# Performance work log

Hardware: AMD Instinct MI355X
Metric: run time of the kernel (lower is better)

The kernel has to match this reference:

```python
import jax, jax.numpy as jnp
import numpy as np

N, D = 8192, 128
WEIGHT = 0.01


def _neg_flat_indices(n):
    # Replicates: mask = ones(n,n); fill_diagonal_(0); mask[i,i+1]=0; mask[i+1,i]=0
    # i.e. keep (i,j) with j != i, j != i+1, j != i-1. Row-major flatnonzero
    # reproduces torch's sim[mask] flattening order exactly.
    i = np.arange(n)[:, None]
    j = np.arange(n)[None, :]
    mask = (j != i) & (j != i + 1) & (j != i - 1)
    idx = np.flatnonzero(mask)
    assert idx.size == (n - 1) * (n - 2)
    return idx


NEG_IDX = jnp.asarray(_neg_flat_indices(N))  # [(N-1)*(N-2)] int32/int64 constant


def setup_inputs() -> dict:
    key = jax.random.key(0)
    factor = jax.random.normal(key, (N, D), dtype=jnp.float32)
    return {"factor": factor}


def reference(factor):
    n = factor.shape[0]
    # F.normalize(factor): L2-normalize rows with eps=1e-12
    norms = jnp.linalg.norm(factor, axis=1, keepdims=True)
    f = factor / jnp.maximum(norms, 1e-12)
    sim = f @ f.T                                   # [N, N] gram matrix
    pos = jnp.diagonal(sim, offset=1).reshape(n - 1, 1)      # [N-1, 1]
    neg = sim.reshape(-1)[NEG_IDX].reshape(n - 1, n - 2)     # [N-1, N-2]
    logits = jnp.concatenate([pos, neg], axis=1)             # [N-1, N-1]
    # CrossEntropyLoss(reduction='sum') with all-zero labels:
    # sum_i (logsumexp(logits_i) - logits_i[0])
    loss = jnp.sum(jax.nn.logsumexp(logits, axis=1) - logits[:, 0])
    loss = loss / n
    return -WEIGHT * loss
```

## Files before the change

### kernel.cpp

```cpp
#include <hip/hip_runtime.h>
#include <hip/hip_bf16.h>

#define N 8192
#define D 128
#define WEIGHT 0.01f
#define NTILES 64
#define NBLK 2080

typedef __bf16 bf16x8 __attribute__((ext_vector_type(8)));
typedef float floatx4 __attribute__((ext_vector_type(4)));

__global__ __launch_bounds__(256) void k_norm(const float* __restrict__ x,
                                              __hip_bfloat16* __restrict__ fb,
                                              float* __restrict__ out) {
    int gid = blockIdx.x * 256 + threadIdx.x;
    if (gid == 0) out[0] = 0.0f;
    int row = gid >> 4;
    int c   = gid & 15;
    const float4* xr = (const float4*)(x + (size_t)row * D + c * 8);
    float4 f0 = xr[0], f1 = xr[1];
    float s = f0.x * f0.x + f0.y * f0.y + f0.z * f0.z + f0.w * f0.w
            + f1.x * f1.x + f1.y * f1.y + f1.z * f1.z + f1.w * f1.w;
    s += __shfl_xor(s, 1, 64);
    s += __shfl_xor(s, 2, 64);
    s += __shfl_xor(s, 4, 64);
    s += __shfl_xor(s, 8, 64);
    float inv = 1.0f / fmaxf(sqrtf(s), 1e-12f);
    union { __hip_bfloat16 h[8]; uint4 u; } pk;
    pk.h[0] = __float2bfloat16(f0.x * inv);
    pk.h[1] = __float2bfloat16(f0.y * inv);
    pk.h[2] = __float2bfloat16(f0.z * inv);
    pk.h[3] = __float2bfloat16(f0.w * inv);
    pk.h[4] = __float2bfloat16(f1.x * inv);
    pk.h[5] = __float2bfloat16(f1.y * inv);
    pk.h[6] = __float2bfloat16(f1.z * inv);
    pk.h[7] = __float2bfloat16(f1.w * inv);
    ((uint4*)fb)[(size_t)row * 16 + (c ^ (row & 15))] = pk.u;
}

__global__ __launch_bounds__(256, 2) void k_gram(const __hip_bfloat16* __restrict__ fb,
                                                 float* __restrict__ Prow,
                                                 float* __restrict__ Pcol,
                                                 float* __restrict__ p,
                                                 float* __restrict__ ep) {
    int b = blockIdx.x;
    int bi = (int)((2.0 * NTILES + 1.0 - sqrt((2.0 * NTILES + 1.0) * (2.0 * NTILES + 1.0) - 8.0 * (double)b)) * 0.5);
    while (bi * NTILES - bi * (bi - 1) / 2 > b) --bi;
    while ((bi + 1) * NTILES - (bi + 1) * bi / 2 <= b) ++bi;
    int bj = bi + (b - (bi * NTILES - bi * (bi - 1) / 2));

    __shared__ uint4 Ab[2048];
    __shared__ uint4 Bb[2048];
    __shared__ float PR[2][128];
    __shared__ float PC[2][128];

    const int t = threadIdx.x;
    const int lane = t & 63;
    const int wid  = t >> 6;
    const int wrow = wid >> 1, wcol = wid & 1;
    const int col0 = lane & 15;
    const int quad = lane >> 4;
    const int rbase = bi * 128, cbase = bj * 128;

    const uint4* gA = (const uint4*)fb + (size_t)rbase * 16;
    const uint4* gB = (const uint4*)fb + (size_t)cbase * 16;
    #pragma unroll
    for (int i = 0; i < 8; ++i) {
        int ca = wid * 512 + i * 64;
        __builtin_amdgcn_global_load_lds(
            (const __attribute__((address_space(1))) void*)(gA + ca + lane),
            (__attribute__((address_space(3))) void*)&Ab[ca], 16, 0, 0);
        __builtin_amdgcn_global_load_lds(
            (const __attribute__((address_space(1))) void*)(gB + ca + lane),
            (__attribute__((address_space(3))) void*)&Bb[ca], 16, 0, 0);
    }
    __syncthreads();

    floatx4 acc[4][4];
    #pragma unroll
    for (int a = 0; a < 4; ++a)
        #pragma unroll
        for (int c = 0; c < 4; ++c)
            acc[a][c] = (floatx4){0.0f, 0.0f, 0.0f, 0.0f};

    #pragma unroll
    for (int ks = 0; ks < 4; ++ks) {
        bf16x8 af[4], bfr[4];
        int j = ks * 4 + quad;
        int jsw = j ^ col0;
        #pragma unroll
        for (int mt = 0; mt < 4; ++mt) {
            int rl = wrow * 64 + mt * 16 + col0;
            af[mt] = *(const bf16x8*)&Ab[rl * 16 + jsw];
        }
        #pragma unroll
        for (int nt = 0; nt < 4; ++nt) {
            int cl = wcol * 64 + nt * 16 + col0;
            bfr[nt] = *(const bf16x8*)&Bb[cl * 16 + jsw];
        }
        #pragma unroll
        for (int mt = 0; mt < 4; ++mt)
            #pragma unroll
            for (int nt = 0; nt < 4; ++nt)
                acc[mt][nt] = __builtin_amdgcn_mfma_f32_16x16x32_bf16(af[mt], bfr[nt], acc[mt][nt], 0, 0, 0);
    }

    float v[16];
    float colpart[4];
    #pragma unroll
    for (int m = 0; m < 16; ++m) v[m] = 0.0f;
    #pragma unroll
    for (int m = 0; m < 4; ++m) colpart[m] = 0.0f;

    if (bj > bi + 1) {
        #pragma unroll
        for (int mt = 0; mt < 4; ++mt)
            #pragma unroll
            for (int nt = 0; nt < 4; ++nt)
                #pragma unroll
                for (int reg = 0; reg < 4; ++reg) {
                    float e = __expf(acc[mt][nt][reg]);
                    v[mt * 4 + reg] += e;
                    colpart[nt] += e;
                }
    } else {
        #pragma unroll
        for (int mt = 0; mt < 4; ++mt)
            #pragma unroll
            for (int nt = 0; nt < 4; ++nt)
                #pragma unroll
                for (int reg = 0; reg < 4; ++reg) {
                    int r = rbase + wrow * 64 + mt * 16 + quad * 4 + reg;
                    int c = cbase + wcol * 64 + nt * 16 + col0;
                    float s0 = acc[mt][nt][reg];
                    float e = __expf(s0);
                    if (c == r + 1) { p[r] = s0; ep[r] = e; }
                    e = (c > r) ? e : 0.0f;
                    v[mt * 4 + reg] += e;
                    colpart[nt] += e;
                }
    }

    float v8[8];
    #pragma unroll
    for (int k = 0; k < 8; ++k) {
        float a = v[2 * k], bb = v[2 * k + 1];
        float give = (lane & 1) ? a : bb;
        float keep = (lane & 1) ? bb : a;
        v8[k] = keep + __shfl_xor(give, 1, 64);
    }
    float v4[4];
    #pragma unroll
    for (int k = 0; k < 4; ++k) {
        float a = v8[2 * k], bb = v8[2 * k + 1];
        float give = (lane & 2) ? a : bb;
        float keep = (lane & 2) ? bb : a;
        v4[k] = keep + __shfl_xor(give, 2, 64);
    }
    float v2[2];
    #pragma unroll
    for (int k = 0; k < 2; ++k) {
        float a = v4[2 * k], bb = v4[2 * k + 1];
        float give = (lane & 4) ? a : bb;
        float keep = (lane & 4) ? bb : a;
        v2[k] = keep + __shfl_xor(give, 4, 64);
    }
    {
        float a = v2[0], bb = v2[1];
        float give = (lane & 8) ? a : bb;
        float keep = (lane & 8) ? bb : a;
        float v1 = keep + __shfl_xor(give, 8, 64);
        int rowl = wrow * 64 + (col0 >> 2) * 16 + quad * 4 + (col0 & 3);
        PR[wcol][rowl] = v1;
    }
    {
        float c2[2];
        #pragma unroll
        for (int k = 0; k < 2; ++k) {
            float a = colpart[2 * k];
            float bb = colpart[2 * k + 1];
            float give = (lane & 16) ? a : bb;
            float keep = (lane & 16) ? bb : a;
            c2[k] = keep + __shfl_xor(give, 16, 64);
        }
        float a = c2[0], bb = c2[1];
        float give = (lane & 32) ? a : bb;
        float keep = (lane & 32) ? bb : a;
        float cv = keep + __shfl_xor(give, 32, 64);
        PC[wrow][wcol * 64 + lane] = cv;
    }
    __syncthreads();

    if (t < 128) {
        Prow[(size_t)b * 128 + t] = PR[0][t] + PR[1][t];
    } else {
        int c = t - 128;
        Pcol[(size_t)b * 128 + c] = PC[0][c] + PC[1][c];
    }
}

__global__ __launch_bounds__(256) void k_tail(const float* __restrict__ Prow,
                                              const float* __restrict__ Pcol,
                                              const float* __restrict__ p,
                                              const float* __restrict__ ep,
                                              float* __restrict__ out) {
    __shared__ float Ush[128];
    __shared__ float Lsh[128];
    __shared__ float sw[4];
    int band = blockIdx.x;
    int t = threadIdx.x;
    if (t < 128) {
        int baseU = band * NTILES - band * (band - 1) / 2;
        float s = 0.0f;
        for (int bj = band; bj < NTILES; ++bj)
            s += Prow[(size_t)(baseU + bj - band) * 128 + t];
        Ush[t] = s;
    } else {
        int c = band * 128 + (t - 128) + 1;
        float s = 0.0f;
        if (c < N) {
            int bc = c >> 7;
            for (int bi = 0; bi <= bc; ++bi)
                s += Pcol[(size_t)(bi * NTILES - bi * (bi - 1) / 2 + (bc - bi)) * 128 + (c & 127)];
        }
        Lsh[t - 128] = s;
    }
    __syncthreads();
    float term = 0.0f;
    if (t < 128) {
        int r = band * 128 + t;
        if (r < N - 1)
            term = __logf(Ush[t] + Lsh[t] - ep[r]) - p[r];
    }
    #pragma unroll
    for (int m = 1; m < 64; m <<= 1) term += __shfl_xor(term, m, 64);
    int lane = t & 63, wd = t >> 6;
    if (lane == 0) sw[wd] = term;
    __syncthreads();
    if (t == 0) {
        float part = sw[0] + sw[1] + sw[2] + sw[3];
        atomicAdd(out, -WEIGHT * part / (float)N);
    }
}

extern "C" void kernel_launch(void* const* d_in, const int* in_sizes, int n_in,
                              void* d_out, int out_size, void* d_ws, size_t ws_size,
                              hipStream_t stream) {
    const float* x = (const float*)d_in[0];
    float* out = (float*)d_out;
    char* ws = (char*)d_ws;
    __hip_bfloat16* fb = (__hip_bfloat16*)ws;
    float* p    = (float*)(ws + (size_t)N * D * 2);
    float* ep   = p + N;
    float* Prow = ep + N;
    float* Pcol = Prow + (size_t)NBLK * 128;

    hipLaunchKernelGGL(k_norm, dim3(512),  dim3(256), 0, stream, x, fb, out);
    hipLaunchKernelGGL(k_gram, dim3(NBLK), dim3(256), 0, stream, fb, Prow, Pcol, p, ep);
    hipLaunchKernelGGL(k_tail, dim3(64),   dim3(256), 0, stream, Prow, Pcol, p, ep, out);
}
```

Before: 95.33 us.

## Fuse tail reduction into gram kernel via atomic ticket and spin barrier

Drops the separate k_tail launch. Each gram block takes an atomic ticket after writing its partials. The last 64 ticket holders wait on a flag set by the final block, then each does one band's reduction and adds to the output. This removes a kernel launch and its gap, at the cost of an atomic per block and spin-waiting blocks, which could delay the final block's scheduling.

```diff
diff --git a/kernel.cpp b/kernel.cpp
--- a/kernel.cpp
+++ b/kernel.cpp
@@ -6,15 +6,17 @@
 #define WEIGHT 0.01f
 #define NTILES 64
 #define NBLK 2080
+#define NTAIL 64
 
 typedef __bf16 bf16x8 __attribute__((ext_vector_type(8)));
 typedef float floatx4 __attribute__((ext_vector_type(4)));
 
 __global__ __launch_bounds__(256) void k_norm(const float* __restrict__ x,
                                               __hip_bfloat16* __restrict__ fb,
-                                              float* __restrict__ out) {
+                                              float* __restrict__ out,
+                                              unsigned* __restrict__ sync) {
     int gid = blockIdx.x * 256 + threadIdx.x;
-    if (gid == 0) out[0] = 0.0f;
+    if (gid == 0) { out[0] = 0.0f; sync[0] = 0u; sync[32] = 0u; }
     int row = gid >> 4;
     int c   = gid & 15;
     const float4* xr = (const float4*)(x + (size_t)row * D + c * 8);
@@ -42,7 +44,9 @@
                                                  float* __restrict__ Prow,
                                                  float* __restrict__ Pcol,
                                                  float* __restrict__ p,
-                                                 float* __restrict__ ep) {
+                                                 float* __restrict__ ep,
+                                                 unsigned* __restrict__ sync,
+                                                 float* __restrict__ out) {
     int b = blockIdx.x;
     int bi = (int)((2.0 * NTILES + 1.0 - sqrt((2.0 * NTILES + 1.0) * (2.0 * NTILES + 1.0) - 8.0 * (double)b)) * 0.5);
     while (bi * NTILES - bi * (bi - 1) / 2 > b) --bi;
@@ -53,6 +57,7 @@
     __shared__ uint4 Bb[2048];
     __shared__ float PR[2][128];
     __shared__ float PC[2][128];
+    __shared__ unsigned ticket_sh;
 
     const int t = threadIdx.x;
     const int lane = t & 63;
@@ -197,49 +202,58 @@
         int c = t - 128;
         Pcol[(size_t)b * 128 + c] = PC[0][c] + PC[1][c];
     }
-}
-
-__global__ __launch_bounds__(256) void k_tail(const float* __restrict__ Prow,
-                                              const float* __restrict__ Pcol,
-                                              const float* __restrict__ p,
-                                              const float* __restrict__ ep,
-                                              float* __restrict__ out) {
-    __shared__ float Ush[128];
-    __shared__ float Lsh[128];
-    __shared__ float sw[4];
-    int band = blockIdx.x;
-    int t = threadIdx.x;
-    if (t < 128) {
-        int baseU = band * NTILES - band * (band - 1) / 2;
-        float s = 0.0f;
-        for (int bj = band; bj < NTILES; ++bj)
-            s += Prow[(size_t)(baseU + bj - band) * 128 + t];
-        Ush[t] = s;
+
+    __threadfence();
+    __syncthreads();
+    if (t == 0)
+        ticket_sh = __hip_atomic_fetch_add(&sync[0], 1u, __ATOMIC_ACQ_REL, __HIP_MEMORY_SCOPE_AGENT);
+    __syncthreads();
+    unsigned ticket = ticket_sh;
+    if (ticket < NBLK - NTAIL) return;
+
+    if (ticket == NBLK - 1) {
+        if (t == 0)
+            __hip_atomic_store(&sync[32], 1u, __ATOMIC_RELEASE, __HIP_MEMORY_SCOPE_AGENT);
     } else {
-        int c = band * 128 + (t - 128) + 1;
-        float s = 0.0f;
-        if (c < N) {
-            int bc = c >> 7;
-            for (int bi = 0; bi <= bc; ++bi)
-                s += Pcol[(size_t)(bi * NTILES - bi * (bi - 1) / 2 + (bc - bi)) * 128 + (c & 127)];
-        }
-        Lsh[t - 128] = s;
-    }
-    __syncthreads();
-    float term = 0.0f;
-    if (t < 128) {
-        int r = band * 128 + t;
-        if (r < N - 1)
-            term = __logf(Ush[t] + Lsh[t] - ep[r]) - p[r];
-    }
-    #pragma unroll
-    for (int m = 1; m < 64; m <<= 1) term += __shfl_xor(term, m, 64);
-    int lane = t & 63, wd = t >> 6;
-    if (lane == 0) sw[wd] = term;
-    __syncthreads();
-    if (t == 0) {
-        float part = sw[0] + sw[1] + sw[2] + sw[3];
-        atomicAdd(out, -WEIGHT * part / (float)N);
+        if (t == 0)
+            while (__hip_atomic_load(&sync[32], __ATOMIC_ACQUIRE, __HIP_MEMORY_SCOPE_AGENT) == 0u)
+                __builtin_amdgcn_s_sleep(4);
+        __syncthreads();
+    }
+
+    {
+        int band = (int)ticket - (NBLK - NTAIL);
+        if (t < 128) {
+            int baseU = band * NTILES - band * (band - 1) / 2;
+            float s = 0.0f;
+            for (int bjj = band; bjj < NTILES; ++bjj)
+                s += Prow[(size_t)(baseU + bjj - band) * 128 + t];
+            PR[0][t] = s;
+        } else {
+            int c = band * 128 + (t - 128) + 1;
+            float s = 0.0f;
+            if (c < N) {
+                int bc = c >> 7;
+                for (int bii = 0; bii <= bc; ++bii)
+                    s += Pcol[(size_t)(bii * NTILES - bii * (bii - 1) / 2 + (bc - bii)) * 128 + (c & 127)];
+            }
+            PR[1][t - 128] = s;
+        }
+        __syncthreads();
+        float term = 0.0f;
+        if (t < 128) {
+            int r = band * 128 + t;
+            if (r < N - 1)
+                term = __logf(PR[0][t] + PR[1][t] - ep[r]) - p[r];
+        }
+        #pragma unroll
+        for (int m = 1; m < 64; m <<= 1) term += __shfl_xor(term, m, 64);
+        if (lane == 0) PC[0][wid] = term;
+        __syncthreads();
+        if (t == 0) {
+            float part = PC[0][0] + PC[0][1] + PC[0][2] + PC[0][3];
+            atomicAdd(out, -WEIGHT * part / (float)N);
+        }
     }
 }
 
@@ -252,10 +266,10 @@
     __hip_bfloat16* fb = (__hip_bfloat16*)ws;
     float* p    = (float*)(ws + (size_t)N * D * 2);
     float* ep   = p + N;
-    float* Prow = ep + N;
+    unsigned* sync = (unsigned*)(ep + N);
+    float* Prow = (float*)(sync + 64);
     float* Pcol = Prow + (size_t)NBLK * 128;
 
-    hipLaunchKernelGGL(k_norm, dim3(512),  dim3(256), 0, stream, x, fb, out);
-    hipLaunchKernelGGL(k_gram, dim3(NBLK), dim3(256), 0, stream, fb, Prow, Pcol, p, ep);
-    hipLaunchKernelGGL(k_tail, dim3(64),   dim3(256), 0, stream, Prow, Pcol, p, ep, out);
+    hipLaunchKernelGGL(k_norm, dim3(512),  dim3(256), 0, stream, x, fb, out, sync);
+    hipLaunchKernelGGL(k_gram, dim3(NBLK), dim3(256), 0, stream, fb, Prow, Pcol, p, ep, sync, out);
 }
```

Result: slower. 271.2 us (+184.5%).

## Switch normalized features and gram MFMA from bf16 to fp8 e4m3

Applied to the files above, without the earlier changes.

Normalized rows are now quantized to fp8 e4m3 instead of bf16, which halves the staged operand bytes and LDS tile size. The gram kernel uses the fp8 16x16x32 MFMA with a new 8-byte swizzle layout, and occupancy is raised to 4 blocks per CU. The aim is to cut MFMA time and memory traffic in the gram stage, at the cost of much lower precision in the similarities that feed exp/logsumexp, which risks failing the accuracy tolerance.

```diff
diff --git a/kernel.cpp b/kernel.cpp
--- a/kernel.cpp
+++ b/kernel.cpp
@@ -1,5 +1,6 @@
 #include <hip/hip_runtime.h>
 #include <hip/hip_bf16.h>
+#include <hip/hip_fp8.h>
 
 #define N 8192
 #define D 128
@@ -7,11 +8,10 @@
 #define NTILES 64
 #define NBLK 2080
 
-typedef __bf16 bf16x8 __attribute__((ext_vector_type(8)));
 typedef float floatx4 __attribute__((ext_vector_type(4)));
 
 __global__ __launch_bounds__(256) void k_norm(const float* __restrict__ x,
-                                              __hip_bfloat16* __restrict__ fb,
+                                              unsigned char* __restrict__ fb8,
                                               float* __restrict__ out) {
     int gid = blockIdx.x * 256 + threadIdx.x;
     if (gid == 0) out[0] = 0.0f;
@@ -26,19 +26,20 @@
     s += __shfl_xor(s, 4, 64);
     s += __shfl_xor(s, 8, 64);
     float inv = 1.0f / fmaxf(sqrtf(s), 1e-12f);
-    union { __hip_bfloat16 h[8]; uint4 u; } pk;
-    pk.h[0] = __float2bfloat16(f0.x * inv);
-    pk.h[1] = __float2bfloat16(f0.y * inv);
-    pk.h[2] = __float2bfloat16(f0.z * inv);
-    pk.h[3] = __float2bfloat16(f0.w * inv);
-    pk.h[4] = __float2bfloat16(f1.x * inv);
-    pk.h[5] = __float2bfloat16(f1.y * inv);
-    pk.h[6] = __float2bfloat16(f1.z * inv);
-    pk.h[7] = __float2bfloat16(f1.w * inv);
-    ((uint4*)fb)[(size_t)row * 16 + (c ^ (row & 15))] = pk.u;
-}
-
-__global__ __launch_bounds__(256, 2) void k_gram(const __hip_bfloat16* __restrict__ fb,
+    union { unsigned char b[8]; uint2 u; } pk;
+    pk.b[0] = __hip_fp8_e4m3(f0.x * inv).__x;
+    pk.b[1] = __hip_fp8_e4m3(f0.y * inv).__x;
+    pk.b[2] = __hip_fp8_e4m3(f0.z * inv).__x;
+    pk.b[3] = __hip_fp8_e4m3(f0.w * inv).__x;
+    pk.b[4] = __hip_fp8_e4m3(f1.x * inv).__x;
+    pk.b[5] = __hip_fp8_e4m3(f1.y * inv).__x;
+    pk.b[6] = __hip_fp8_e4m3(f1.z * inv).__x;
+    pk.b[7] = __hip_fp8_e4m3(f1.w * inv).__x;
+    int cc = c >> 1, h = c & 1;
+    ((uint2*)fb8)[(size_t)row * 16 + (((cc ^ (row & 7)) << 1) | h)] = pk.u;
+}
+
+__global__ __launch_bounds__(256, 4) void k_gram(const unsigned char* __restrict__ fb8,
                                                  float* __restrict__ Prow,
                                                  float* __restrict__ Pcol,
                                                  float* __restrict__ p,
@@ -49,8 +50,8 @@
     while ((bi + 1) * NTILES - (bi + 1) * bi / 2 <= b) ++bi;
     int bj = bi + (b - (bi * NTILES - bi * (bi - 1) / 2));
 
-    __shared__ uint4 Ab[2048];
-    __shared__ uint4 Bb[2048];
+    __shared__ uint4 Ab[1024];
+    __shared__ uint4 Bb[1024];
     __shared__ float PR[2][128];
     __shared__ float PC[2][128];
 
@@ -62,11 +63,11 @@
     const int quad = lane >> 4;
     const int rbase = bi * 128, cbase = bj * 128;
 
-    const uint4* gA = (const uint4*)fb + (size_t)rbase * 16;
-    const uint4* gB = (const uint4*)fb + (size_t)cbase * 16;
-    #pragma unroll
-    for (int i = 0; i < 8; ++i) {
-        int ca = wid * 512 + i * 64;
+    const uint4* gA = (const uint4*)fb8 + (size_t)rbase * 8;
+    const uint4* gB = (const uint4*)fb8 + (size_t)cbase * 8;
+    #pragma unroll
+    for (int i = 0; i < 4; ++i) {
+        int ca = wid * 256 + i * 64;
         __builtin_amdgcn_global_load_lds(
             (const __attribute__((address_space(1))) void*)(gA + ca + lane),
             (__attribute__((address_space(3))) void*)&Ab[ca], 16, 0, 0);
@@ -83,26 +84,30 @@
         for (int c = 0; c < 4; ++c)
             acc[a][c] = (floatx4){0.0f, 0.0f, 0.0f, 0.0f};
 
+    const long* A8 = (const long*)Ab;
+    const long* B8 = (const long*)Bb;
+    const int swz = (col0 & 7);
     #pragma unroll
     for (int ks = 0; ks < 4; ++ks) {
-        bf16x8 af[4], bfr[4];
-        int j = ks * 4 + quad;
-        int jsw = j ^ col0;
+        long af[4], bfr[4];
+        int cc = ks * 2 + (quad >> 1);
+        int off = quad & 1;
+        int base8 = ((cc ^ swz) << 1) | off;
         #pragma unroll
         for (int mt = 0; mt < 4; ++mt) {
             int rl = wrow * 64 + mt * 16 + col0;
-            af[mt] = *(const bf16x8*)&Ab[rl * 16 + jsw];
+            af[mt] = A8[rl * 16 + base8];
         }
         #pragma unroll
         for (int nt = 0; nt < 4; ++nt) {
             int cl = wcol * 64 + nt * 16 + col0;
-            bfr[nt] = *(const bf16x8*)&Bb[cl * 16 + jsw];
+            bfr[nt] = B8[cl * 16 + base8];
         }
         #pragma unroll
         for (int mt = 0; mt < 4; ++mt)
             #pragma unroll
             for (int nt = 0; nt < 4; ++nt)
-                acc[mt][nt] = __builtin_amdgcn_mfma_f32_16x16x32_bf16(af[mt], bfr[nt], acc[mt][nt], 0, 0, 0);
+                acc[mt][nt] = __builtin_amdgcn_mfma_f32_16x16x32_fp8_fp8(af[mt], bfr[nt], acc[mt][nt], 0, 0, 0);
     }
 
     float v[16];
@@ -249,13 +254,13 @@
     const float* x = (const float*)d_in[0];
     float* out = (float*)d_out;
     char* ws = (char*)d_ws;
-    __hip_bfloat16* fb = (__hip_bfloat16*)ws;
-    float* p    = (float*)(ws + (size_t)N * D * 2);
+    unsigned char* fb8 = (unsigned char*)ws;
+    float* p    = (float*)(ws + (size_t)N * D);
     float* ep   = p + N;
     float* Prow = ep + N;
     float* Pcol = Prow + (size_t)NBLK * 128;
 
-    hipLaunchKernelGGL(k_norm, dim3(512),  dim3(256), 0, stream, x, fb, out);
-    hipLaunchKernelGGL(k_gram, dim3(NBLK), dim3(256), 0, stream, fb, Prow, Pcol, p, ep);
+    hipLaunchKernelGGL(k_norm, dim3(512),  dim3(256), 0, stream, x, fb8, out);
+    hipLaunchKernelGGL(k_gram, dim3(NBLK), dim3(256), 0, stream, fb8, Prow, Pcol, p, ep);
     hipLaunchKernelGGL(k_tail, dim3(64),   dim3(256), 0, stream, Prow, Pcol, p, ep, out);
 }
```

Result: faster. 91.59 us (-3.9%).
